# Kernel optimization log

Hardware: AMD Instinct MI355X
Metric: run time of the kernel (lower is better)

The kernel has to match this reference:

```python
import jax, jax.numpy as jnp
import numpy as np

C = 64; H = 80; W = 160; B = 3; L = 4
REC = [4, 3, 2]  # agents per scene, sum = 9
EPS = 1e-5
NEG = -1e30  # stands in for -inf (numerically identical after softmax)


def setup_inputs() -> dict:
    key = jax.random.key(0)
    ks = jax.random.split(key, 24)
    def p(i, shape, s=0.05):
        return s * jax.random.normal(ks[i], shape, jnp.float32)
    x = jax.random.normal(ks[0], (sum(REC), C, H, W), jnp.float32)
    mask = jnp.ones((B, L, H, W), jnp.float32)
    record_len = jnp.array(REC, jnp.int32)
    eye = jnp.broadcast_to(jnp.array([[1., 0., 0.], [0., 1., 0.]], jnp.float32), (B, L, L, 2, 3))
    noise = 0.05 * jax.random.normal(ks[1], (B, L, L, 2, 3), jnp.float32)
    diag = jnp.eye(L, dtype=bool)[None, :, :, None, None]
    pairwise_t_matrix = jnp.where(diag, eye, eye + noise)  # near-identity normalized affines
    inp = dict(x=x, mask=mask, record_len=record_len, pairwise_t_matrix=pairwise_t_matrix)
    chans = [(2 * C, 128), (128, 32), (32, 8)]
    for n, (ci, co) in zip([1, 2, 3], chans):
        inp[f'w{n}'] = p(2 * n, (ci, co))
        inp[f'cb{n}'] = p(2 * n + 1, (co,), 0.01)
        inp[f'g{n}'] = 1.0 + p(8 + n, (co,), 0.1)
        inp[f'be{n}'] = p(12 + n, (co,), 0.1)
        inp[f'rm{n}'] = jnp.zeros((co,), jnp.float32)
        inp[f'rv{n}'] = jnp.ones((co,), jnp.float32)
    inp['w4'] = p(16, (8, 1)); inp['cb4'] = p(17, (1,), 0.01)
    inp['mlp_w'] = p(18, (C, C)); inp['mlp_b'] = p(19, (C,), 0.01)
    return inp


def _bilinear(feat, px, py):
    # feat [C,H,W]; px,py [H,W] source pixel coords; zero padding outside
    x0 = jnp.floor(px); y0 = jnp.floor(py)
    wx = px - x0; wy = py - y0
    x0i = x0.astype(jnp.int32); y0i = y0.astype(jnp.int32)
    def gat(xi, yi):
        inb = ((xi >= 0) & (xi < W) & (yi >= 0) & (yi < H)).astype(feat.dtype)
        v = feat[:, jnp.clip(yi, 0, H - 1), jnp.clip(xi, 0, W - 1)]
        return v * inb
    return (gat(x0i, y0i) * (1 - wx) * (1 - wy) + gat(x0i + 1, y0i) * wx * (1 - wy)
            + gat(x0i, y0i + 1) * (1 - wx) * wy + gat(x0i + 1, y0i + 1) * wx * wy)


def _warp_one(feat, theta):
    # torch affine_grid convention: src_norm = theta @ [x_n, y_n, 1]
    ys = jnp.linspace(-1.0, 1.0, H); xs = jnp.linspace(-1.0, 1.0, W)
    gx, gy = jnp.meshgrid(xs, ys)  # [H,W]
    sx = theta[0, 0] * gx + theta[0, 1] * gy + theta[0, 2]
    sy = theta[1, 0] * gx + theta[1, 1] * gy + theta[1, 2]
    px = (sx + 1.0) * (W - 1) / 2.0
    py = (sy + 1.0) * (H - 1) / 2.0
    return _bilinear(feat, px, py)

_warp_j = jax.vmap(_warp_one, in_axes=(0, 0))        # over neighbor j
_warp_ij = jax.vmap(_warp_j, in_axes=(None, 0))      # over ego i
_warp_bij = jax.vmap(_warp_ij, in_axes=(0, 0))       # over scene b


def _forward(x, mask, rec, ptm, w1, cb1, g1, be1, rm1, rv1, w2, cb2, g2, be2, rm2, rv2,
             w3, cb3, g3, be3, rm3, rv3, w4, cb4, mlp_w, mlp_b):
    # regroup: pad per-scene agent features to [B,L,C,H,W]
    feats, idx = [], 0
    for n in rec:
        feats.append(jnp.pad(x[idx:idx + n], ((0, L - n), (0, 0), (0, 0), (0, 0))))
        idx += n
    node = jnp.stack(feats)                                      # [B,L,C,H,W]
    valid = jnp.asarray((np.asarray(rec)[:, None] > np.arange(L)).astype(np.float32))  # [B,L]
    theta = jnp.swapaxes(ptm, 1, 2)                              # theta[b,i,j] = ptm[b,j,i]
    nbr = _warp_bij(node, theta)                                 # [B,L,L,C,H,W]
    wm = _warp_bij(mask[:, :, None], theta)                      # [B,L,L,1,H,W] warped ROI masks
    com_mask = wm * valid[:, None, :, None, None, None]
    ego = jnp.broadcast_to(node[:, :, None], nbr.shape)          # ego feature repeated over j
    z = jnp.concatenate([nbr, ego], axis=3)                      # [B,L,L,2C,H,W]

    def conv_bn_relu(t, w, cb, g, be, rm, rv):
        t = jnp.einsum('bijchw,co->bijohw', t, w) + cb[:, None, None]
        t = (t - rm[:, None, None]) * (g[:, None, None] / jnp.sqrt(rv[:, None, None] + EPS)) + be[:, None, None]
        return jax.nn.relu(t)

    h = conv_bn_relu(z, w1, cb1, g1, be1, rm1, rv1)
    h = conv_bn_relu(h, w2, cb2, g2, be2, rm2, rv2)
    h = conv_bn_relu(h, w3, cb3, g3, be3, rm3, rv3)
    s = jax.nn.relu(jnp.einsum('bijchw,co->bijohw', h, w4) + cb4[:, None, None])  # [B,L,L,1,H,W]
    s = jnp.where(com_mask == 0, NEG, s)
    aw = jax.nn.softmax(s, axis=2)                               # softmax over neighbors j
    updated = jnp.sum(aw * nbr * com_mask, axis=2)               # [B,L,C,H,W]
    out = updated[:, 0]                                          # ego agent per scene [B,C,H,W]
    return jnp.einsum('bchw,cd->bdhw', out, mlp_w) + mlp_b[:, None, None]


def reference(x, mask, record_len, pairwise_t_matrix, w1, cb1, g1, be1, rm1, rv1,
              w2, cb2, g2, be2, rm2, rv2, w3, cb3, g3, be3, rm3, rv3, w4, cb4, mlp_w, mlp_b):
    rec = [int(v) for v in np.asarray(record_len)]
    return _forward(x, mask, rec, pairwise_t_matrix, w1, cb1, g1, be1, rm1, rv1,
                    w2, cb2, g2, be2, rm2, rv2, w3, cb3, g3, be3, rm3, rv3, w4, cb4, mlp_w, mlp_b)
```

## Files before the change

kernel.cpp:

```cpp
#include <hip/hip_runtime.h>
#include <math.h>

#define CC 64
#define HH 80
#define WW 160
#define BB 3
#define LL 4
#define HW (HH * WW)
#define EPSf 1e-5f
#define NEGf -1e30f

typedef __attribute__((ext_vector_type(8))) short bf16x8;
typedef __attribute__((ext_vector_type(4))) float f32x4;

__device__ __forceinline__ unsigned short f2bf(float f) {
    unsigned int u = __float_as_uint(f);
    u = u + 0x7fffu + ((u >> 16) & 1u);
    return (unsigned short)(u >> 16);
}
__device__ __forceinline__ float b2f(unsigned short h) {
    return __uint_as_float(((unsigned int)h) << 16);
}

__device__ __forceinline__ void src_xy(const float* __restrict__ th, int pix,
                                       float& px, float& py) {
    int w = pix % WW, h = pix / WW;
    float gx = -1.f + 2.f * (float)w / (float)(WW - 1);
    float gy = -1.f + 2.f * (float)h / (float)(HH - 1);
    float sx = th[0] * gx + th[1] * gy + th[2];
    float sy = th[3] * gx + th[4] * gy + th[5];
    px = (sx + 1.f) * (float)(WW - 1) * 0.5f;
    py = (sy + 1.f) * (float)(HH - 1) * 0.5f;
}


__global__ __launch_bounds__(256) void k_prep(
    const float* __restrict__ w1, const float* __restrict__ w2,
    const float* __restrict__ cb1, const float* __restrict__ g1,
    const float* __restrict__ be1, const float* __restrict__ rm1, const float* __restrict__ rv1,
    const float* __restrict__ cb2, const float* __restrict__ g2,
    const float* __restrict__ be2, const float* __restrict__ rm2, const float* __restrict__ rv2,
    const float* __restrict__ cb3, const float* __restrict__ g3,
    const float* __restrict__ be3, const float* __restrict__ rm3, const float* __restrict__ rv3,
    unsigned short* __restrict__ w1T, unsigned short* __restrict__ w2T,
    float* __restrict__ kk1, float* __restrict__ bb1,
    float* __restrict__ kk2, float* __restrict__ bb2,
    float* __restrict__ kk3, float* __restrict__ bb3)
{
    int idx = blockIdx.x * 256 + threadIdx.x;
    if (idx < 16384) {
        int o = idx >> 7, c = idx & 127;
        w1T[idx] = f2bf(w1[c * 128 + o]);
    } else if (idx < 20480) {
        int i = idx - 16384;
        int o2 = i >> 7, o = i & 127;
        w2T[i] = f2bf(w2[o * 32 + o2]);
    } else if (idx < 20608) {
        int o = idx - 20480;
        float k = g1[o] * rsqrtf(rv1[o] + EPSf);
        kk1[o] = k; bb1[o] = fmaf(cb1[o] - rm1[o], k, be1[o]);
    } else if (idx < 20640) {
        int o = idx - 20608;
        float k = g2[o] * rsqrtf(rv2[o] + EPSf);
        kk2[o] = k; bb2[o] = fmaf(cb2[o] - rm2[o], k, be2[o]);
    } else if (idx < 20648) {
        int o = idx - 20640;
        float k = g3[o] * rsqrtf(rv3[o] + EPSf);
        kk3[o] = k; bb3[o] = fmaf(cb3[o] - rm3[o], k, be3[o]);
    }
}


__global__ __launch_bounds__(256) void k_warp(
    const float* __restrict__ x, const float* __restrict__ mask,
    const int* __restrict__ rec, const float* __restrict__ ptm,
    unsigned short* __restrict__ nbr_t, unsigned short* __restrict__ ego_t,
    float* __restrict__ com)
{
    __shared__ unsigned short tile_s[64 * 72];
    int bid = blockIdx.x, t = threadIdx.x;
    int p = t & 63, cg = t >> 6;
    int r0 = rec[0], r1 = rec[1], r2 = rec[2];

    if (bid < 2400) {
        int bj = bid / 200, tile = bid % 200;
        int b = bj >> 2, j = bj & 3;
        int rb = (b == 0) ? r0 : ((b == 1) ? r1 : r2);
        int pix0 = tile * 64;
        if (j >= rb) {
            if (t < 64) com[(size_t)bj * HW + pix0 + t] = 0.f;
            return;
        }
        int off = (b >= 1 ? r0 : 0) + (b >= 2 ? r1 : 0);
        const float* th = ptm + ((size_t)(b * 4 + j) * 4 + 0) * 6;
        int pix = pix0 + p;
        float px, py; src_xy(th, pix, px, py);
        float x0f = floorf(px), y0f = floorf(py);
        float wx = px - x0f, wy = py - y0f;
        int x0 = (int)x0f, y0 = (int)y0f, x1 = x0 + 1, y1 = y0 + 1;
        float bx0 = (x0 >= 0 && x0 < WW) ? 1.f : 0.f;
        float bx1 = (x1 >= 0 && x1 < WW) ? 1.f : 0.f;
        float by0 = (y0 >= 0 && y0 < HH) ? 1.f : 0.f;
        float by1 = (y1 >= 0 && y1 < HH) ? 1.f : 0.f;
        int xc0 = min(max(x0, 0), WW - 1), xc1 = min(max(x1, 0), WW - 1);
        int yc0 = min(max(y0, 0), HH - 1), yc1 = min(max(y1, 0), HH - 1);
        float w00 = (1.f - wx) * (1.f - wy) * bx0 * by0;
        float w01 = wx * (1.f - wy) * bx1 * by0;
        float w10 = (1.f - wx) * wy * bx0 * by1;
        float w11 = wx * wy * bx1 * by1;
        int a00 = yc0 * WW + xc0, a01 = yc0 * WW + xc1;
        int a10 = yc1 * WW + xc0, a11 = yc1 * WW + xc1;
        const float* feat = x + (size_t)(off + j) * CC * HW;
        #pragma unroll
        for (int i = 0; i < 16; ++i) {
            int c = cg * 16 + i;
            const float* f = feat + (size_t)c * HW;
            float v = w00 * f[a00] + w01 * f[a01] + w10 * f[a10] + w11 * f[a11];
            tile_s[p * 72 + c] = f2bf(v);
        }
        if (t < 64) {
            const float* mk = mask + (size_t)(b * 4 + j) * HW;
            float wm = w00 * mk[a00] + w01 * mk[a01] + w10 * mk[a10] + w11 * mk[a11];
            com[(size_t)bj * HW + pix0 + t] = wm;
        }
        __syncthreads();
        unsigned short* dst = nbr_t + ((size_t)bj * HW + pix0) * 64;
        #pragma unroll
        for (int i = 0; i < 2; ++i) {
            int u = i * 256 + t; int pr = u >> 3, cu = u & 7;
            *(uint4*)(dst + pr * 64 + cu * 8) = *(const uint4*)&tile_s[pr * 72 + cu * 8];
        }
    } else {
        int eb = bid - 2400;
        int b = eb / 200, tile = eb % 200, pix0 = tile * 64;
        int off = (b >= 1 ? r0 : 0) + (b >= 2 ? r1 : 0);
        const float* feat = x + (size_t)off * CC * HW;
        #pragma unroll
        for (int i = 0; i < 16; ++i) {
            int c = cg * 16 + i;
            tile_s[p * 72 + c] = f2bf(feat[(size_t)c * HW + pix0 + p]);
        }
        __syncthreads();
        unsigned short* dst = ego_t + ((size_t)b * HW + pix0) * 64;
        #pragma unroll
        for (int i = 0; i < 2; ++i) {
            int u = i * 256 + t; int pr = u >> 3, cu = u & 7;
            *(uint4*)(dst + pr * 64 + cu * 8) = *(const uint4*)&tile_s[pr * 72 + cu * 8];
        }
    }
}


__global__ __launch_bounds__(256) void k_score(
    const unsigned short* __restrict__ nbr_t, const unsigned short* __restrict__ ego_t,
    const unsigned short* __restrict__ w1T, const unsigned short* __restrict__ w2T,
    const float* __restrict__ kk1, const float* __restrict__ bb1,
    const float* __restrict__ kk2, const float* __restrict__ bb2,
    const float* __restrict__ kk3, const float* __restrict__ bb3,
    const float* __restrict__ w3, const float* __restrict__ w4,
    const float* __restrict__ cb4, const int* __restrict__ rec,
    float* __restrict__ s_out)
{
    __shared__ unsigned short Zs[128 * 136];
    __shared__ float H2f[128 * 36];
    int bid = blockIdx.x, t = threadIdx.x;
    int bj = bid / 100, tile = bid % 100;
    int b = bj >> 2, j = bj & 3;
    int r0 = rec[0], r1 = rec[1], r2 = rec[2];
    int rb = (b == 0) ? r0 : ((b == 1) ? r1 : r2);
    if (j >= rb) return;
    int pix0 = tile * 128;

    const uint4* srcN = (const uint4*)(nbr_t + ((size_t)bj * HW + pix0) * 64);
    const uint4* srcE = (const uint4*)(ego_t + ((size_t)b * HW + pix0) * 64);
    #pragma unroll
    for (int i = 0; i < 4; ++i) {
        int u = i * 256 + t, p = u >> 3, cu = u & 7;
        *(uint4*)&Zs[p * 136 + cu * 8]      = srcN[u];
        *(uint4*)&Zs[p * 136 + 64 + cu * 8] = srcE[u];
    }
    __syncthreads();

    int lane = t & 63, wave = t >> 6;
    int r16 = lane & 15, q = lane >> 4;
    int wbase = wave * 32;
    const f32x4 z4 = {0.f, 0.f, 0.f, 0.f};

    f32x4 acc[2][8];
    #pragma unroll
    for (int mt = 0; mt < 2; ++mt)
        #pragma unroll
        for (int nt = 0; nt < 8; ++nt) acc[mt][nt] = z4;

    #pragma unroll
    for (int ks = 0; ks < 4; ++ks) {
        int kcol = ks * 32 + q * 8;
        bf16x8 a0 = *(const bf16x8*)&Zs[(wbase + r16) * 136 + kcol];
        bf16x8 a1 = *(const bf16x8*)&Zs[(wbase + 16 + r16) * 136 + kcol];
        #pragma unroll
        for (int nt = 0; nt < 8; ++nt) {
            bf16x8 bf = *(const bf16x8*)(w1T + (nt * 16 + r16) * 128 + kcol);
            acc[0][nt] = __builtin_amdgcn_mfma_f32_16x16x32_bf16(a0, bf, acc[0][nt], 0, 0, 0);
            acc[1][nt] = __builtin_amdgcn_mfma_f32_16x16x32_bf16(a1, bf, acc[1][nt], 0, 0, 0);
        }
    }
    #pragma unroll
    for (int nt = 0; nt < 8; ++nt) {
        int o = nt * 16 + r16;
        float kv = kk1[o], bv = bb1[o];
        #pragma unroll
        for (int mt = 0; mt < 2; ++mt) {
            #pragma unroll
            for (int r = 0; r < 4; ++r) {
                float h = fmaxf(fmaf(acc[mt][nt][r], kv, bv), 0.f);
                int row = wbase + mt * 16 + q * 4 + r;
                Zs[row * 136 + o] = f2bf(h);
            }
        }
    }

    f32x4 acc2[2][2];
    acc2[0][0] = z4; acc2[0][1] = z4; acc2[1][0] = z4; acc2[1][1] = z4;
    #pragma unroll
    for (int ks = 0; ks < 4; ++ks) {
        int kcol = ks * 32 + q * 8;
        bf16x8 a0 = *(const bf16x8*)&Zs[(wbase + r16) * 136 + kcol];
        bf16x8 a1 = *(const bf16x8*)&Zs[(wbase + 16 + r16) * 136 + kcol];
        #pragma unroll
        for (int nt = 0; nt < 2; ++nt) {
            bf16x8 bf = *(const bf16x8*)(w2T + (nt * 16 + r16) * 128 + kcol);
            acc2[0][nt] = __builtin_amdgcn_mfma_f32_16x16x32_bf16(a0, bf, acc2[0][nt], 0, 0, 0);
            acc2[1][nt] = __builtin_amdgcn_mfma_f32_16x16x32_bf16(a1, bf, acc2[1][nt], 0, 0, 0);
        }
    }
    #pragma unroll
    for (int nt = 0; nt < 2; ++nt) {
        int o2 = nt * 16 + r16;
        float kv = kk2[o2], bv = bb2[o2];
        #pragma unroll
        for (int mt = 0; mt < 2; ++mt) {
            #pragma unroll
            for (int r = 0; r < 4; ++r) {
                float h = fmaxf(fmaf(acc2[mt][nt][r], kv, bv), 0.f);
                int row = wbase + mt * 16 + q * 4 + r;
                H2f[row * 36 + o2] = h;
            }
        }
    }
    __syncthreads();

    if (t < 128) {
        float h2v[32];
        const float4* hp = (const float4*)&H2f[t * 36];
        #pragma unroll
        for (int qq = 0; qq < 8; ++qq) {
            float4 v = hp[qq];
            h2v[qq * 4 + 0] = v.x; h2v[qq * 4 + 1] = v.y;
            h2v[qq * 4 + 2] = v.z; h2v[qq * 4 + 3] = v.w;
        }
        float a3[8];
        #pragma unroll
        for (int o = 0; o < 8; ++o) a3[o] = 0.f;
        #pragma unroll
        for (int c = 0; c < 32; ++c) {
            #pragma unroll
            for (int o = 0; o < 8; ++o) a3[o] = fmaf(h2v[c], w3[c * 8 + o], a3[o]);
        }
        float s = cb4[0];
        #pragma unroll
        for (int o = 0; o < 8; ++o) {
            float h = fmaxf(fmaf(a3[o], kk3[o], bb3[o]), 0.f);
            s = fmaf(h, w4[o], s);
        }
        s = fmaxf(s, 0.f);
        s_out[(size_t)bj * HW + pix0 + t] = s;
    }
}


__global__ __launch_bounds__(256) void k_fuse(
    const unsigned short* __restrict__ nbr_t, const float* __restrict__ s_in,
    const float* __restrict__ com_in, const float* __restrict__ mlp_w,
    const float* __restrict__ mlp_b, float* __restrict__ out)
{
    __shared__ float s_s[256], com_s[256], wgt_s[256];
    __shared__ float updT[64 * 66];
    __shared__ float w_s[64 * 64];
    int bid = blockIdx.x, t = threadIdx.x;
    int b = bid / 200, tile = bid % 200, pix0 = tile * 64;
    int p = t & 63, cg = t >> 6;

    {
        int jj = t >> 6;
        size_t g = ((size_t)(b * 4 + jj)) * HW + pix0 + (t & 63);
        s_s[t] = s_in[g];
        com_s[t] = com_in[g];
    }
    #pragma unroll
    for (int i = 0; i < 16; ++i) w_s[i * 256 + t] = mlp_w[i * 256 + t];
    __syncthreads();

    if (t < 64) {
        float sj[LL], cj[LL];
        #pragma unroll
        for (int j2 = 0; j2 < LL; ++j2) {
            cj[j2] = com_s[j2 * 64 + t];
            float sv = s_s[j2 * 64 + t];
            sj[j2] = (cj[j2] == 0.f) ? NEGf : sv;
        }
        float m = fmaxf(fmaxf(sj[0], sj[1]), fmaxf(sj[2], sj[3]));
        float e[LL], sum = 0.f;
        #pragma unroll
        for (int j2 = 0; j2 < LL; ++j2) { e[j2] = __expf(sj[j2] - m); sum += e[j2]; }
        float inv = 1.f / sum;
        #pragma unroll
        for (int j2 = 0; j2 < LL; ++j2) wgt_s[j2 * 64 + t] = e[j2] * inv * cj[j2];
    }
    __syncthreads();

    {
        float upd[16];
        #pragma unroll
        for (int i = 0; i < 16; ++i) upd[i] = 0.f;
        #pragma unroll
        for (int jj = 0; jj < LL; ++jj) {
            float wj = wgt_s[jj * 64 + p];
            const unsigned short* nr =
                nbr_t + ((size_t)(b * 4 + jj) * HW + pix0 + p) * 64 + cg * 16;
            uint4 v0 = *(const uint4*)nr;
            uint4 v1 = *(const uint4*)(nr + 8);
            unsigned int uu[8] = {v0.x, v0.y, v0.z, v0.w, v1.x, v1.y, v1.z, v1.w};
            #pragma unroll
            for (int k = 0; k < 8; ++k) {
                float lo = __uint_as_float(uu[k] << 16);
                float hi = __uint_as_float(uu[k] & 0xffff0000u);
                upd[k * 2 + 0] = fmaf(wj, lo, upd[k * 2 + 0]);
                upd[k * 2 + 1] = fmaf(wj, hi, upd[k * 2 + 1]);
            }
        }
        #pragma unroll
        for (int i = 0; i < 16; ++i) updT[(cg * 16 + i) * 66 + p] = upd[i];
    }
    __syncthreads();

    {
        int d0 = cg * 16;
        float acc[16];
        #pragma unroll
        for (int dd = 0; dd < 16; ++dd) acc[dd] = mlp_b[d0 + dd];
        #pragma unroll 4
        for (int c = 0; c < 64; ++c) {
            float u = updT[c * 66 + p];
            const float4* wp = (const float4*)&w_s[c * 64 + d0];
            float4 w0 = wp[0], w1v = wp[1], w2v = wp[2], w3v = wp[3];
            acc[0]  = fmaf(u, w0.x,  acc[0]);  acc[1]  = fmaf(u, w0.y,  acc[1]);
            acc[2]  = fmaf(u, w0.z,  acc[2]);  acc[3]  = fmaf(u, w0.w,  acc[3]);
            acc[4]  = fmaf(u, w1v.x, acc[4]);  acc[5]  = fmaf(u, w1v.y, acc[5]);
            acc[6]  = fmaf(u, w1v.z, acc[6]);  acc[7]  = fmaf(u, w1v.w, acc[7]);
            acc[8]  = fmaf(u, w2v.x, acc[8]);  acc[9]  = fmaf(u, w2v.y, acc[9]);
            acc[10] = fmaf(u, w2v.z, acc[10]); acc[11] = fmaf(u, w2v.w, acc[11]);
            acc[12] = fmaf(u, w3v.x, acc[12]); acc[13] = fmaf(u, w3v.y, acc[13]);
            acc[14] = fmaf(u, w3v.z, acc[14]); acc[15] = fmaf(u, w3v.w, acc[15]);
        }
        #pragma unroll
        for (int dd = 0; dd < 16; ++dd)
            out[((size_t)(b * CC) + d0 + dd) * HW + pix0 + p] = acc[dd];
    }
}


extern "C" void kernel_launch(void* const* d_in, const int* in_sizes, int n_in,
                              void* d_out, int out_size, void* d_ws, size_t ws_size,
                              hipStream_t stream)
{
    const float* x    = (const float*)d_in[0];
    const float* mask = (const float*)d_in[1];
    const int*   rec  = (const int*)  d_in[2];
    const float* ptm  = (const float*)d_in[3];
    const float* w1   = (const float*)d_in[4];
    const float* cb1  = (const float*)d_in[5];
    const float* g1   = (const float*)d_in[6];
    const float* be1  = (const float*)d_in[7];
    const float* rm1  = (const float*)d_in[8];
    const float* rv1  = (const float*)d_in[9];
    const float* w2   = (const float*)d_in[10];
    const float* cb2  = (const float*)d_in[11];
    const float* g2   = (const float*)d_in[12];
    const float* be2  = (const float*)d_in[13];
    const float* rm2  = (const float*)d_in[14];
    const float* rv2  = (const float*)d_in[15];
    const float* w3   = (const float*)d_in[16];
    const float* cb3  = (const float*)d_in[17];
    const float* g3   = (const float*)d_in[18];
    const float* be3  = (const float*)d_in[19];
    const float* rm3  = (const float*)d_in[20];
    const float* rv3  = (const float*)d_in[21];
    const float* w4   = (const float*)d_in[22];
    const float* cb4  = (const float*)d_in[23];
    const float* mlpw = (const float*)d_in[24];
    const float* mlpb = (const float*)d_in[25];
    float* out = (float*)d_out;

    unsigned short* nbr_t = (unsigned short*)d_ws;
    unsigned short* ego_t = nbr_t + (size_t)12 * HW * 64;
    float* s_ws   = (float*)(ego_t + (size_t)3 * HW * 64);
    float* com_ws = s_ws + (size_t)12 * HW;
    unsigned short* w1T = (unsigned short*)(com_ws + (size_t)12 * HW);
    unsigned short* w2T = w1T + 16384;
    float* kk1 = (float*)(w2T + 4096);
    float* bb1 = kk1 + 128;
    float* kk2 = bb1 + 128;
    float* bb2 = kk2 + 32;
    float* kk3 = bb2 + 32;
    float* bb3 = kk3 + 8;

    k_prep<<<dim3(81), dim3(256), 0, stream>>>(
        w1, w2, cb1, g1, be1, rm1, rv1, cb2, g2, be2, rm2, rv2,
        cb3, g3, be3, rm3, rv3, w1T, w2T, kk1, bb1, kk2, bb2, kk3, bb3);

    k_warp<<<dim3(3000), dim3(256), 0, stream>>>(
        x, mask, rec, ptm, nbr_t, ego_t, com_ws);

    k_score<<<dim3(1200), dim3(256), 0, stream>>>(
        nbr_t, ego_t, w1T, w2T, kk1, bb1, kk2, bb2, kk3, bb3,
        w3, w4, cb4, rec, s_ws);

    k_fuse<<<dim3(600), dim3(256), 0, stream>>>(
        nbr_t, s_ws, com_ws, mlpw, mlpb, out);
}
```

Baseline: 181.2 us.

## Fuse warp, scoring MLP, softmax fusion and output projection into one kernel

Replaces the separate warp, score and fuse kernels with one kernel per (scene, 64-pixel tile). It warps each neighbour's features straight into MFMA A-fragments held in registers and runs the 1x1 conv stack with the ego features. It then does the softmax-weighted sum and the output MLP on bf16 MFMA. This removes the large bf16 neighbour/ego workspace round trips through global memory and two kernel launches. In exchange there are fewer blocks (600), a serial loop over neighbours with block barriers, and only 64 threads working during the conv3/score step. The final MLP now runs in bf16 rather than fp32, which adds some precision loss.

```diff
diff --git a/kernel.cpp b/kernel.cpp
--- a/kernel.cpp
+++ b/kernel.cpp
@@ -12,6 +12,8 @@
 
 typedef __attribute__((ext_vector_type(8))) short bf16x8;
 typedef __attribute__((ext_vector_type(4))) float f32x4;
+
+union BU { unsigned short s[8]; bf16x8 v; };
 
 __device__ __forceinline__ unsigned short f2bf(float f) {
     unsigned int u = __float_as_uint(f);
@@ -33,9 +35,32 @@
     py = (sy + 1.f) * (float)(HH - 1) * 0.5f;
 }
 
+struct Tap { int a00, a01, a10, a11; float w00, w01, w10, w11; };
+
+__device__ __forceinline__ Tap mk_tap(float px, float py) {
+    Tap tp;
+    float x0f = floorf(px), y0f = floorf(py);
+    float wx = px - x0f, wy = py - y0f;
+    int x0 = (int)x0f, y0 = (int)y0f, x1 = x0 + 1, y1 = y0 + 1;
+    float bx0 = (x0 >= 0 && x0 < WW) ? 1.f : 0.f;
+    float bx1 = (x1 >= 0 && x1 < WW) ? 1.f : 0.f;
+    float by0 = (y0 >= 0 && y0 < HH) ? 1.f : 0.f;
+    float by1 = (y1 >= 0 && y1 < HH) ? 1.f : 0.f;
+    int xc0 = min(max(x0, 0), WW - 1), xc1 = min(max(x1, 0), WW - 1);
+    int yc0 = min(max(y0, 0), HH - 1), yc1 = min(max(y1, 0), HH - 1);
+    tp.w00 = (1.f - wx) * (1.f - wy) * bx0 * by0;
+    tp.w01 = wx * (1.f - wy) * bx1 * by0;
+    tp.w10 = (1.f - wx) * wy * bx0 * by1;
+    tp.w11 = wx * wy * bx1 * by1;
+    tp.a00 = yc0 * WW + xc0; tp.a01 = yc0 * WW + xc1;
+    tp.a10 = yc1 * WW + xc0; tp.a11 = yc1 * WW + xc1;
+    return tp;
+}
+
 
 __global__ __launch_bounds__(256) void k_prep(
     const float* __restrict__ w1, const float* __restrict__ w2,
+    const float* __restrict__ mlpw,
     const float* __restrict__ cb1, const float* __restrict__ g1,
     const float* __restrict__ be1, const float* __restrict__ rm1, const float* __restrict__ rv1,
     const float* __restrict__ cb2, const float* __restrict__ g2,
@@ -43,6 +68,7 @@
     const float* __restrict__ cb3, const float* __restrict__ g3,
     const float* __restrict__ be3, const float* __restrict__ rm3, const float* __restrict__ rv3,
     unsigned short* __restrict__ w1T, unsigned short* __restrict__ w2T,
+    unsigned short* __restrict__ mwT,
     float* __restrict__ kk1, float* __restrict__ bb1,
     float* __restrict__ kk2, float* __restrict__ bb2,
     float* __restrict__ kk3, float* __restrict__ bb3)
@@ -55,316 +81,236 @@
         int i = idx - 16384;
         int o2 = i >> 7, o = i & 127;
         w2T[i] = f2bf(w2[o * 32 + o2]);
-    } else if (idx < 20608) {
-        int o = idx - 20480;
+    } else if (idx < 24576) {
+        int i = idx - 20480;
+        int d = i >> 6, c = i & 63;
+        mwT[i] = f2bf(mlpw[c * 64 + d]);
+    } else if (idx < 24704) {
+        int o = idx - 24576;
         float k = g1[o] * rsqrtf(rv1[o] + EPSf);
         kk1[o] = k; bb1[o] = fmaf(cb1[o] - rm1[o], k, be1[o]);
-    } else if (idx < 20640) {
-        int o = idx - 20608;
+    } else if (idx < 24736) {
+        int o = idx - 24704;
         float k = g2[o] * rsqrtf(rv2[o] + EPSf);
         kk2[o] = k; bb2[o] = fmaf(cb2[o] - rm2[o], k, be2[o]);
-    } else if (idx < 20648) {
-        int o = idx - 20640;
+    } else if (idx < 24744) {
+        int o = idx - 24736;
         float k = g3[o] * rsqrtf(rv3[o] + EPSf);
         kk3[o] = k; bb3[o] = fmaf(cb3[o] - rm3[o], k, be3[o]);
     }
 }
 
 
-__global__ __launch_bounds__(256) void k_warp(
+__global__ __launch_bounds__(256, 2) void k_fused(
     const float* __restrict__ x, const float* __restrict__ mask,
     const int* __restrict__ rec, const float* __restrict__ ptm,
-    unsigned short* __restrict__ nbr_t, unsigned short* __restrict__ ego_t,
-    float* __restrict__ com)
-{
-    __shared__ unsigned short tile_s[64 * 72];
-    int bid = blockIdx.x, t = threadIdx.x;
-    int p = t & 63, cg = t >> 6;
-    int r0 = rec[0], r1 = rec[1], r2 = rec[2];
-
-    if (bid < 2400) {
-        int bj = bid / 200, tile = bid % 200;
-        int b = bj >> 2, j = bj & 3;
-        int rb = (b == 0) ? r0 : ((b == 1) ? r1 : r2);
-        int pix0 = tile * 64;
-        if (j >= rb) {
-            if (t < 64) com[(size_t)bj * HW + pix0 + t] = 0.f;
-            return;
-        }
-        int off = (b >= 1 ? r0 : 0) + (b >= 2 ? r1 : 0);
-        const float* th = ptm + ((size_t)(b * 4 + j) * 4 + 0) * 6;
-        int pix = pix0 + p;
-        float px, py; src_xy(th, pix, px, py);
-        float x0f = floorf(px), y0f = floorf(py);
-        float wx = px - x0f, wy = py - y0f;
-        int x0 = (int)x0f, y0 = (int)y0f, x1 = x0 + 1, y1 = y0 + 1;
-        float bx0 = (x0 >= 0 && x0 < WW) ? 1.f : 0.f;
-        float bx1 = (x1 >= 0 && x1 < WW) ? 1.f : 0.f;
-        float by0 = (y0 >= 0 && y0 < HH) ? 1.f : 0.f;
-        float by1 = (y1 >= 0 && y1 < HH) ? 1.f : 0.f;
-        int xc0 = min(max(x0, 0), WW - 1), xc1 = min(max(x1, 0), WW - 1);
-        int yc0 = min(max(y0, 0), HH - 1), yc1 = min(max(y1, 0), HH - 1);
-        float w00 = (1.f - wx) * (1.f - wy) * bx0 * by0;
-        float w01 = wx * (1.f - wy) * bx1 * by0;
-        float w10 = (1.f - wx) * wy * bx0 * by1;
-        float w11 = wx * wy * bx1 * by1;
-        int a00 = yc0 * WW + xc0, a01 = yc0 * WW + xc1;
-        int a10 = yc1 * WW + xc0, a11 = yc1 * WW + xc1;
-        const float* feat = x + (size_t)(off + j) * CC * HW;
-        #pragma unroll
-        for (int i = 0; i < 16; ++i) {
-            int c = cg * 16 + i;
-            const float* f = feat + (size_t)c * HW;
-            float v = w00 * f[a00] + w01 * f[a01] + w10 * f[a10] + w11 * f[a11];
-            tile_s[p * 72 + c] = f2bf(v);
-        }
-        if (t < 64) {
-            const float* mk = mask + (size_t)(b * 4 + j) * HW;
-            float wm = w00 * mk[a00] + w01 * mk[a01] + w10 * mk[a10] + w11 * mk[a11];
-            com[(size_t)bj * HW + pix0 + t] = wm;
-        }
-        __syncthreads();
-        unsigned short* dst = nbr_t + ((size_t)bj * HW + pix0) * 64;
-        #pragma unroll
-        for (int i = 0; i < 2; ++i) {
-            int u = i * 256 + t; int pr = u >> 3, cu = u & 7;
-            *(uint4*)(dst + pr * 64 + cu * 8) = *(const uint4*)&tile_s[pr * 72 + cu * 8];
-        }
-    } else {
-        int eb = bid - 2400;
-        int b = eb / 200, tile = eb % 200, pix0 = tile * 64;
-        int off = (b >= 1 ? r0 : 0) + (b >= 2 ? r1 : 0);
-        const float* feat = x + (size_t)off * CC * HW;
-        #pragma unroll
-        for (int i = 0; i < 16; ++i) {
-            int c = cg * 16 + i;
-            tile_s[p * 72 + c] = f2bf(feat[(size_t)c * HW + pix0 + p]);
-        }
-        __syncthreads();
-        unsigned short* dst = ego_t + ((size_t)b * HW + pix0) * 64;
-        #pragma unroll
-        for (int i = 0; i < 2; ++i) {
-            int u = i * 256 + t; int pr = u >> 3, cu = u & 7;
-            *(uint4*)(dst + pr * 64 + cu * 8) = *(const uint4*)&tile_s[pr * 72 + cu * 8];
-        }
-    }
-}
-
-
-__global__ __launch_bounds__(256) void k_score(
-    const unsigned short* __restrict__ nbr_t, const unsigned short* __restrict__ ego_t,
     const unsigned short* __restrict__ w1T, const unsigned short* __restrict__ w2T,
+    const unsigned short* __restrict__ mwT,
     const float* __restrict__ kk1, const float* __restrict__ bb1,
     const float* __restrict__ kk2, const float* __restrict__ bb2,
     const float* __restrict__ kk3, const float* __restrict__ bb3,
     const float* __restrict__ w3, const float* __restrict__ w4,
-    const float* __restrict__ cb4, const int* __restrict__ rec,
-    float* __restrict__ s_out)
+    const float* __restrict__ cb4, const float* __restrict__ mlp_b,
+    float* __restrict__ out)
 {
-    __shared__ unsigned short Zs[128 * 136];
-    __shared__ float H2f[128 * 36];
-    int bid = blockIdx.x, t = threadIdx.x;
-    int bj = bid / 100, tile = bid % 100;
-    int b = bj >> 2, j = bj & 3;
+    __shared__ unsigned short H1s[64 * 136];
+    __shared__ float H2f[64 * 36];
+    __shared__ float s_s[4 * 64];
+    __shared__ float com_s[4 * 64];
+
+    int t = threadIdx.x;
+    int b = blockIdx.x / 200, tile = blockIdx.x % 200;
+    int pix0 = tile * 64;
+    int wave = t >> 6, lane = t & 63, q = lane >> 4, r16 = lane & 15;
+    int p = wave * 16 + r16;
+    int pix = pix0 + p;
+
     int r0 = rec[0], r1 = rec[1], r2 = rec[2];
     int rb = (b == 0) ? r0 : ((b == 1) ? r1 : r2);
-    if (j >= rb) return;
-    int pix0 = tile * 128;
-
-    const uint4* srcN = (const uint4*)(nbr_t + ((size_t)bj * HW + pix0) * 64);
-    const uint4* srcE = (const uint4*)(ego_t + ((size_t)b * HW + pix0) * 64);
-    #pragma unroll
-    for (int i = 0; i < 4; ++i) {
-        int u = i * 256 + t, p = u >> 3, cu = u & 7;
-        *(uint4*)&Zs[p * 136 + cu * 8]      = srcN[u];
-        *(uint4*)&Zs[p * 136 + 64 + cu * 8] = srcE[u];
+    int off = (b >= 1 ? r0 : 0) + (b >= 2 ? r1 : 0);
+
+    float kv1[8], bv1[8];
+    #pragma unroll
+    for (int nt = 0; nt < 8; ++nt) { int o = nt * 16 + r16; kv1[nt] = kk1[o]; bv1[nt] = bb1[o]; }
+    float kv2[2], bv2[2];
+    #pragma unroll
+    for (int nt = 0; nt < 2; ++nt) { int o = nt * 16 + r16; kv2[nt] = kk2[o]; bv2[nt] = bb2[o]; }
+
+    bf16x8 e0, e1;
+    {
+        BU u0, u1;
+        const float* xe = x + (size_t)off * CC * HW + pix;
+        #pragma unroll
+        for (int i = 0; i < 8; ++i) {
+            u0.s[i] = f2bf(xe[(size_t)(q * 8 + i) * HW]);
+            u1.s[i] = f2bf(xe[(size_t)(32 + q * 8 + i) * HW]);
+        }
+        e0 = u0.v; e1 = u1.v;
+    }
+
+    const f32x4 z4 = {0.f, 0.f, 0.f, 0.f};
+    bf16x8 nbrA[8];
+
+    #pragma unroll
+    for (int j = 0; j < 4; ++j) {
+        bf16x8 a0 = {0,0,0,0,0,0,0,0}, a1 = {0,0,0,0,0,0,0,0};
+        bool valid = j < rb;
+        if (valid) {
+            const float* th = ptm + ((size_t)(b * 4 + j) * 4) * 6;
+            float px, py; src_xy(th, pix, px, py);
+            Tap tp = mk_tap(px, py);
+            const float* feat = x + (size_t)(off + j) * CC * HW;
+            BU u0, u1;
+            #pragma unroll
+            for (int i = 0; i < 8; ++i) {
+                const float* f0 = feat + (size_t)(q * 8 + i) * HW;
+                float v0 = tp.w00 * f0[tp.a00] + tp.w01 * f0[tp.a01]
+                         + tp.w10 * f0[tp.a10] + tp.w11 * f0[tp.a11];
+                u0.s[i] = f2bf(v0);
+                const float* f1 = feat + (size_t)(32 + q * 8 + i) * HW;
+                float v1 = tp.w00 * f1[tp.a00] + tp.w01 * f1[tp.a01]
+                         + tp.w10 * f1[tp.a10] + tp.w11 * f1[tp.a11];
+                u1.s[i] = f2bf(v1);
+            }
+            a0 = u0.v; a1 = u1.v;
+
+            f32x4 acc1[8];
+            #pragma unroll
+            for (int nt = 0; nt < 8; ++nt) acc1[nt] = z4;
+            #pragma unroll
+            for (int ks = 0; ks < 4; ++ks) {
+                bf16x8 A = (ks == 0) ? a0 : (ks == 1) ? a1 : (ks == 2) ? e0 : e1;
+                int kcol = ks * 32 + q * 8;
+                #pragma unroll
+                for (int nt = 0; nt < 8; ++nt) {
+                    bf16x8 bf = *(const bf16x8*)(w1T + (size_t)(nt * 16 + r16) * 128 + kcol);
+                    acc1[nt] = __builtin_amdgcn_mfma_f32_16x16x32_bf16(A, bf, acc1[nt], 0, 0, 0);
+                }
+            }
+            #pragma unroll
+            for (int nt = 0; nt < 8; ++nt) {
+                #pragma unroll
+                for (int r = 0; r < 4; ++r) {
+                    float h = fmaxf(fmaf(acc1[nt][r], kv1[nt], bv1[nt]), 0.f);
+                    H1s[(wave * 16 + q * 4 + r) * 136 + nt * 16 + r16] = f2bf(h);
+                }
+            }
+            f32x4 acc2[2]; acc2[0] = z4; acc2[1] = z4;
+            #pragma unroll
+            for (int ks = 0; ks < 4; ++ks) {
+                int kcol = ks * 32 + q * 8;
+                bf16x8 A = *(const bf16x8*)&H1s[(wave * 16 + r16) * 136 + kcol];
+                #pragma unroll
+                for (int nt = 0; nt < 2; ++nt) {
+                    bf16x8 bf = *(const bf16x8*)(w2T + (size_t)(nt * 16 + r16) * 128 + kcol);
+                    acc2[nt] = __builtin_amdgcn_mfma_f32_16x16x32_bf16(A, bf, acc2[nt], 0, 0, 0);
+                }
+            }
+            #pragma unroll
+            for (int nt = 0; nt < 2; ++nt) {
+                #pragma unroll
+                for (int r = 0; r < 4; ++r) {
+                    float h = fmaxf(fmaf(acc2[nt][r], kv2[nt], bv2[nt]), 0.f);
+                    H2f[(wave * 16 + q * 4 + r) * 36 + nt * 16 + r16] = h;
+                }
+            }
+        }
+        __syncthreads();
+        if (t < 64) {
+            if (valid) {
+                const float* th = ptm + ((size_t)(b * 4 + j) * 4) * 6;
+                float px, py; src_xy(th, pix0 + t, px, py);
+                Tap tp = mk_tap(px, py);
+                const float* mk = mask + (size_t)(b * 4 + j) * HW;
+                float wm = tp.w00 * mk[tp.a00] + tp.w01 * mk[tp.a01]
+                         + tp.w10 * mk[tp.a10] + tp.w11 * mk[tp.a11];
+                float a3[8];
+                #pragma unroll
+                for (int o = 0; o < 8; ++o) a3[o] = 0.f;
+                #pragma unroll 4
+                for (int c = 0; c < 32; ++c) {
+                    float hv = H2f[t * 36 + c];
+                    #pragma unroll
+                    for (int o = 0; o < 8; ++o) a3[o] = fmaf(hv, w3[c * 8 + o], a3[o]);
+                }
+                float s = cb4[0];
+                #pragma unroll
+                for (int o = 0; o < 8; ++o) {
+                    float h = fmaxf(fmaf(a3[o], kk3[o], bb3[o]), 0.f);
+                    s = fmaf(h, w4[o], s);
+                }
+                s = fmaxf(s, 0.f);
+                s_s[j * 64 + t] = (wm == 0.f) ? NEGf : s;
+                com_s[j * 64 + t] = wm;
+            } else {
+                s_s[j * 64 + t] = NEGf;
+                com_s[j * 64 + t] = 0.f;
+            }
+        }
+        __syncthreads();
+        nbrA[j * 2 + 0] = a0;
+        nbrA[j * 2 + 1] = a1;
+    }
+
+    float sj[4], cj[4];
+    #pragma unroll
+    for (int j = 0; j < 4; ++j) { sj[j] = s_s[j * 64 + p]; cj[j] = com_s[j * 64 + p]; }
+    float m = fmaxf(fmaxf(sj[0], sj[1]), fmaxf(sj[2], sj[3]));
+    float e[4], sum = 0.f;
+    #pragma unroll
+    for (int j = 0; j < 4; ++j) { e[j] = __expf(sj[j] - m); sum += e[j]; }
+    float inv = 1.f / sum;
+    float wgt[4];
+    #pragma unroll
+    for (int j = 0; j < 4; ++j) wgt[j] = e[j] * inv * cj[j];
+
+    float u0f[8], u1f[8];
+    #pragma unroll
+    for (int i = 0; i < 8; ++i) { u0f[i] = 0.f; u1f[i] = 0.f; }
+    #pragma unroll
+    for (int j = 0; j < 4; ++j) {
+        float wj = wgt[j];
+        #pragma unroll
+        for (int i = 0; i < 8; ++i) {
+            u0f[i] = fmaf(wj, b2f((unsigned short)nbrA[j * 2 + 0][i]), u0f[i]);
+            u1f[i] = fmaf(wj, b2f((unsigned short)nbrA[j * 2 + 1][i]), u1f[i]);
+        }
+    }
+    BU p0, p1;
+    #pragma unroll
+    for (int i = 0; i < 8; ++i) { p0.s[i] = f2bf(u0f[i]); p1.s[i] = f2bf(u1f[i]); }
+
+    f32x4 acc3[4];
+    #pragma unroll
+    for (int nt = 0; nt < 4; ++nt) acc3[nt] = z4;
+    #pragma unroll
+    for (int ks = 0; ks < 2; ++ks) {
+        bf16x8 A = ks ? p1.v : p0.v;
+        int kcol = ks * 32 + q * 8;
+        #pragma unroll
+        for (int nt = 0; nt < 4; ++nt) {
+            bf16x8 bf = *(const bf16x8*)(mwT + (size_t)(nt * 16 + r16) * 64 + kcol);
+            acc3[nt] = __builtin_amdgcn_mfma_f32_16x16x32_bf16(A, bf, acc3[nt], 0, 0, 0);
+        }
+    }
+
+    float* outT = (float*)H1s;
+    #pragma unroll
+    for (int nt = 0; nt < 4; ++nt) {
+        int d = nt * 16 + r16;
+        float mb = mlp_b[d];
+        #pragma unroll
+        for (int r = 0; r < 4; ++r)
+            outT[d * 65 + wave * 16 + q * 4 + r] = acc3[nt][r] + mb;
     }
     __syncthreads();
-
-    int lane = t & 63, wave = t >> 6;
-    int r16 = lane & 15, q = lane >> 4;
-    int wbase = wave * 32;
-    const f32x4 z4 = {0.f, 0.f, 0.f, 0.f};
-
-    f32x4 acc[2][8];
-    #pragma unroll
-    for (int mt = 0; mt < 2; ++mt)
-        #pragma unroll
-        for (int nt = 0; nt < 8; ++nt) acc[mt][nt] = z4;
-
-    #pragma unroll
-    for (int ks = 0; ks < 4; ++ks) {
-        int kcol = ks * 32 + q * 8;
-        bf16x8 a0 = *(const bf16x8*)&Zs[(wbase + r16) * 136 + kcol];
-        bf16x8 a1 = *(const bf16x8*)&Zs[(wbase + 16 + r16) * 136 + kcol];
-        #pragma unroll
-        for (int nt = 0; nt < 8; ++nt) {
-            bf16x8 bf = *(const bf16x8*)(w1T + (nt * 16 + r16) * 128 + kcol);
-            acc[0][nt] = __builtin_amdgcn_mfma_f32_16x16x32_bf16(a0, bf, acc[0][nt], 0, 0, 0);
-            acc[1][nt] = __builtin_amdgcn_mfma_f32_16x16x32_bf16(a1, bf, acc[1][nt], 0, 0, 0);
-        }
-    }
-    #pragma unroll
-    for (int nt = 0; nt < 8; ++nt) {
-        int o = nt * 16 + r16;
-        float kv = kk1[o], bv = bb1[o];
-        #pragma unroll
-        for (int mt = 0; mt < 2; ++mt) {
-            #pragma unroll
-            for (int r = 0; r < 4; ++r) {
-                float h = fmaxf(fmaf(acc[mt][nt][r], kv, bv), 0.f);
-                int row = wbase + mt * 16 + q * 4 + r;
-                Zs[row * 136 + o] = f2bf(h);
-            }
-        }
-    }
-
-    f32x4 acc2[2][2];
-    acc2[0][0] = z4; acc2[0][1] = z4; acc2[1][0] = z4; acc2[1][1] = z4;
-    #pragma unroll
-    for (int ks = 0; ks < 4; ++ks) {
-        int kcol = ks * 32 + q * 8;
-        bf16x8 a0 = *(const bf16x8*)&Zs[(wbase + r16) * 136 + kcol];
-        bf16x8 a1 = *(const bf16x8*)&Zs[(wbase + 16 + r16) * 136 + kcol];
-        #pragma unroll
-        for (int nt = 0; nt < 2; ++nt) {
-            bf16x8 bf = *(const bf16x8*)(w2T + (nt * 16 + r16) * 128 + kcol);
-            acc2[0][nt] = __builtin_amdgcn_mfma_f32_16x16x32_bf16(a0, bf, acc2[0][nt], 0, 0, 0);
-            acc2[1][nt] = __builtin_amdgcn_mfma_f32_16x16x32_bf16(a1, bf, acc2[1][nt], 0, 0, 0);
-        }
-    }
-    #pragma unroll
-    for (int nt = 0; nt < 2; ++nt) {
-        int o2 = nt * 16 + r16;
-        float kv = kk2[o2], bv = bb2[o2];
-        #pragma unroll
-        for (int mt = 0; mt < 2; ++mt) {
-            #pragma unroll
-            for (int r = 0; r < 4; ++r) {
-                float h = fmaxf(fmaf(acc2[mt][nt][r], kv, bv), 0.f);
-                int row = wbase + mt * 16 + q * 4 + r;
-                H2f[row * 36 + o2] = h;
-            }
-        }
-    }
-    __syncthreads();
-
-    if (t < 128) {
-        float h2v[32];
-        const float4* hp = (const float4*)&H2f[t * 36];
-        #pragma unroll
-        for (int qq = 0; qq < 8; ++qq) {
-            float4 v = hp[qq];
-            h2v[qq * 4 + 0] = v.x; h2v[qq * 4 + 1] = v.y;
-            h2v[qq * 4 + 2] = v.z; h2v[qq * 4 + 3] = v.w;
-        }
-        float a3[8];
-        #pragma unroll
-        for (int o = 0; o < 8; ++o) a3[o] = 0.f;
-        #pragma unroll
-        for (int c = 0; c < 32; ++c) {
-            #pragma unroll
-            for (int o = 0; o < 8; ++o) a3[o] = fmaf(h2v[c], w3[c * 8 + o], a3[o]);
-        }
-        float s = cb4[0];
-        #pragma unroll
-        for (int o = 0; o < 8; ++o) {
-            float h = fmaxf(fmaf(a3[o], kk3[o], bb3[o]), 0.f);
-            s = fmaf(h, w4[o], s);
-        }
-        s = fmaxf(s, 0.f);
-        s_out[(size_t)bj * HW + pix0 + t] = s;
-    }
-}
-
-
-__global__ __launch_bounds__(256) void k_fuse(
-    const unsigned short* __restrict__ nbr_t, const float* __restrict__ s_in,
-    const float* __restrict__ com_in, const float* __restrict__ mlp_w,
-    const float* __restrict__ mlp_b, float* __restrict__ out)
-{
-    __shared__ float s_s[256], com_s[256], wgt_s[256];
-    __shared__ float updT[64 * 66];
-    __shared__ float w_s[64 * 64];
-    int bid = blockIdx.x, t = threadIdx.x;
-    int b = bid / 200, tile = bid % 200, pix0 = tile * 64;
-    int p = t & 63, cg = t >> 6;
-
     {
-        int jj = t >> 6;
-        size_t g = ((size_t)(b * 4 + jj)) * HW + pix0 + (t & 63);
-        s_s[t] = s_in[g];
-        com_s[t] = com_in[g];
-    }
-    #pragma unroll
-    for (int i = 0; i < 16; ++i) w_s[i * 256 + t] = mlp_w[i * 256 + t];
-    __syncthreads();
-
-    if (t < 64) {
-        float sj[LL], cj[LL];
-        #pragma unroll
-        for (int j2 = 0; j2 < LL; ++j2) {
-            cj[j2] = com_s[j2 * 64 + t];
-            float sv = s_s[j2 * 64 + t];
-            sj[j2] = (cj[j2] == 0.f) ? NEGf : sv;
-        }
-        float m = fmaxf(fmaxf(sj[0], sj[1]), fmaxf(sj[2], sj[3]));
-        float e[LL], sum = 0.f;
-        #pragma unroll
-        for (int j2 = 0; j2 < LL; ++j2) { e[j2] = __expf(sj[j2] - m); sum += e[j2]; }
-        float inv = 1.f / sum;
-        #pragma unroll
-        for (int j2 = 0; j2 < LL; ++j2) wgt_s[j2 * 64 + t] = e[j2] * inv * cj[j2];
-    }
-    __syncthreads();
-
-    {
-        float upd[16];
-        #pragma unroll
-        for (int i = 0; i < 16; ++i) upd[i] = 0.f;
-        #pragma unroll
-        for (int jj = 0; jj < LL; ++jj) {
-            float wj = wgt_s[jj * 64 + p];
-            const unsigned short* nr =
-                nbr_t + ((size_t)(b * 4 + jj) * HW + pix0 + p) * 64 + cg * 16;
-            uint4 v0 = *(const uint4*)nr;
-            uint4 v1 = *(const uint4*)(nr + 8);
-            unsigned int uu[8] = {v0.x, v0.y, v0.z, v0.w, v1.x, v1.y, v1.z, v1.w};
-            #pragma unroll
-            for (int k = 0; k < 8; ++k) {
-                float lo = __uint_as_float(uu[k] << 16);
-                float hi = __uint_as_float(uu[k] & 0xffff0000u);
-                upd[k * 2 + 0] = fmaf(wj, lo, upd[k * 2 + 0]);
-                upd[k * 2 + 1] = fmaf(wj, hi, upd[k * 2 + 1]);
-            }
-        }
-        #pragma unroll
-        for (int i = 0; i < 16; ++i) updT[(cg * 16 + i) * 66 + p] = upd[i];
-    }
-    __syncthreads();
-
-    {
-        int d0 = cg * 16;
-        float acc[16];
-        #pragma unroll
-        for (int dd = 0; dd < 16; ++dd) acc[dd] = mlp_b[d0 + dd];
-        #pragma unroll 4
-        for (int c = 0; c < 64; ++c) {
-            float u = updT[c * 66 + p];
-            const float4* wp = (const float4*)&w_s[c * 64 + d0];
-            float4 w0 = wp[0], w1v = wp[1], w2v = wp[2], w3v = wp[3];
-            acc[0]  = fmaf(u, w0.x,  acc[0]);  acc[1]  = fmaf(u, w0.y,  acc[1]);
-            acc[2]  = fmaf(u, w0.z,  acc[2]);  acc[3]  = fmaf(u, w0.w,  acc[3]);
-            acc[4]  = fmaf(u, w1v.x, acc[4]);  acc[5]  = fmaf(u, w1v.y, acc[5]);
-            acc[6]  = fmaf(u, w1v.z, acc[6]);  acc[7]  = fmaf(u, w1v.w, acc[7]);
-            acc[8]  = fmaf(u, w2v.x, acc[8]);  acc[9]  = fmaf(u, w2v.y, acc[9]);
-            acc[10] = fmaf(u, w2v.z, acc[10]); acc[11] = fmaf(u, w2v.w, acc[11]);
-            acc[12] = fmaf(u, w3v.x, acc[12]); acc[13] = fmaf(u, w3v.y, acc[13]);
-            acc[14] = fmaf(u, w3v.z, acc[14]); acc[15] = fmaf(u, w3v.w, acc[15]);
-        }
-        #pragma unroll
-        for (int dd = 0; dd < 16; ++dd)
-            out[((size_t)(b * CC) + d0 + dd) * HW + pix0 + p] = acc[dd];
+        int p2 = t & 63, dg = t >> 6;
+        #pragma unroll
+        for (int i = 0; i < 16; ++i) {
+            int d = dg * 16 + i;
+            out[((size_t)(b * CC + d)) * HW + pix0 + p2] = outT[d * 65 + p2];
+        }
     }
 }
 
@@ -401,30 +347,22 @@
     const float* mlpb = (const float*)d_in[25];
     float* out = (float*)d_out;
 
-    unsigned short* nbr_t = (unsigned short*)d_ws;
-    unsigned short* ego_t = nbr_t + (size_t)12 * HW * 64;
-    float* s_ws   = (float*)(ego_t + (size_t)3 * HW * 64);
-    float* com_ws = s_ws + (size_t)12 * HW;
-    unsigned short* w1T = (unsigned short*)(com_ws + (size_t)12 * HW);
+    unsigned short* w1T = (unsigned short*)d_ws;
     unsigned short* w2T = w1T + 16384;
-    float* kk1 = (float*)(w2T + 4096);
+    unsigned short* mwT = w2T + 4096;
+    float* kk1 = (float*)(mwT + 4096);
     float* bb1 = kk1 + 128;
     float* kk2 = bb1 + 128;
     float* bb2 = kk2 + 32;
     float* kk3 = bb2 + 32;
     float* bb3 = kk3 + 8;
 
-    k_prep<<<dim3(81), dim3(256), 0, stream>>>(
-        w1, w2, cb1, g1, be1, rm1, rv1, cb2, g2, be2, rm2, rv2,
-        cb3, g3, be3, rm3, rv3, w1T, w2T, kk1, bb1, kk2, bb2, kk3, bb3);
-
-    k_warp<<<dim3(3000), dim3(256), 0, stream>>>(
-        x, mask, rec, ptm, nbr_t, ego_t, com_ws);
-
-    k_score<<<dim3(1200), dim3(256), 0, stream>>>(
-        nbr_t, ego_t, w1T, w2T, kk1, bb1, kk2, bb2, kk3, bb3,
-        w3, w4, cb4, rec, s_ws);
-
-    k_fuse<<<dim3(600), dim3(256), 0, stream>>>(
-        nbr_t, s_ws, com_ws, mlpw, mlpb, out);
-}
+    k_prep<<<dim3(97), dim3(256), 0, stream>>>(
+        w1, w2, mlpw, cb1, g1, be1, rm1, rv1, cb2, g2, be2, rm2, rv2,
+        cb3, g3, be3, rm3, rv3, w1T, w2T, mwT, kk1, bb1, kk2, bb2, kk3, bb3);
+
+    k_fused<<<dim3(600), dim3(256), 0, stream>>>(
+        x, mask, rec, ptm, w1T, w2T, mwT,
+        kk1, bb1, kk2, bb2, kk3, bb3,
+        w3, w4, cb4, mlpb, out);
+}
```

After: 177.1 us. 2.2% less time.
